# Performance work log

Hardware: AMD Instinct MI355X
Metric: run time of the kernel (lower is better)

## Reference

```python
import jax, jax.numpy as jnp
import numpy as np

N_BODIES = 3
NDOF = 3 * N_BODIES          # 9
HIDDEN = 128                 # max(16, 256//2)
EPS2 = 0.1 ** 2              # softening_eps^2
MASS_EPS = 1e-8
B = 262144
# torch.triu_indices(3, 3, 1) -> pairs (0,1),(0,2),(1,2)
PAIR_I = jnp.array([0, 0, 1])
PAIR_J = jnp.array([1, 2, 2])


def setup_inputs() -> dict:
    key = jax.random.key(0)
    ks = jax.random.split(key, 7)
    inv = lambda n: 1.0 / np.sqrt(n)  # torch Linear default init scale (uniform bound)
    return {
        "z": jax.random.normal(ks[0], (B, 2 * NDOF), jnp.float32),
        "log_m_body": jnp.zeros((N_BODIES,), jnp.float32),
        "W1": jax.random.uniform(ks[1], (HIDDEN, 1), jnp.float32, -inv(1), inv(1)),
        "b1": jax.random.uniform(ks[2], (HIDDEN,), jnp.float32, -inv(1), inv(1)),
        "W2": jax.random.uniform(ks[3], (HIDDEN, HIDDEN), jnp.float32, -inv(HIDDEN), inv(HIDDEN)),
        "b2": jax.random.uniform(ks[4], (HIDDEN,), jnp.float32, -inv(HIDDEN), inv(HIDDEN)),
        "W3": jax.random.uniform(ks[5], (1, HIDDEN), jnp.float32, -inv(HIDDEN), inv(HIDDEN)),
        "b3": jax.random.uniform(ks[6], (1,), jnp.float32, -inv(HIDDEN), inv(HIDDEN)),
    }


def _hamiltonian(z, log_m_body, W1, b1, W2, b2, W3, b3):
    q, p = z[:, :NDOF], z[:, NDOF:]
    # kinetic: T(p) = 0.5 * sum p^2 / m  (tied per-body learned mass)
    minv = 1.0 / (jnp.repeat(jnp.exp(log_m_body), 3) + MASS_EPS)  # [ndof]
    T = 0.5 * jnp.sum(p * p * minv, axis=1)                        # [B]
    # potential: softened inverse pairwise distance -> tiny MLP -> sum over pairs
    qb = q.reshape(-1, N_BODIES, 3)
    diff = qb[:, PAIR_I] - qb[:, PAIR_J]                           # [B,3,3]
    d = jnp.sqrt(jnp.sum(diff * diff, axis=-1) + EPS2)             # [B,3]
    s = (1.0 / d)[..., None]                                       # [B,3,1]
    h = jax.nn.silu(s @ W1.T + b1)                                 # [B,3,128]
    h = jax.nn.silu(h @ W2.T + b2)                                 # [B,3,128]
    v = (h @ W3.T + b3)[..., 0]                                    # [B,3]
    V = jnp.sum(v, axis=1)                                         # [B]
    return T + V


def reference(z, log_m_body, W1, b1, W2, b2, W3, b3):
    # dz/dt = J grad_z H with canonical J: dq/dt = dH/dp, dp/dt = -dH/dq
    grad = jax.grad(
        lambda zz: jnp.sum(_hamiltonian(zz, log_m_body, W1, b1, W2, b2, W3, b3))
    )(z)
    dqdt = grad[:, NDOF:]
    dpdt = -grad[:, :NDOF]
    return jnp.concatenate([dqdt, dpdt], axis=1)
```

## Files before the change

kernel.cpp:

```cpp
#include <hip/hip_runtime.h>
#include <math.h>

#define HIDDEN      128
#define TABLE_N     2048
#define SMAX        10.0f
#define E           8
#define TB_THREADS  128
#define MAIN_THREADS 256
#define EPS2        0.01f
#define MASS_EPS    1e-8f

__global__ __launch_bounds__(TB_THREADS)
void build_table_kernel(const float* __restrict__ W1,
                        const float* __restrict__ b1,
                        const float* __restrict__ W2,
                        const float* __restrict__ b2,
                        const float* __restrict__ W3,
                        float* __restrict__ table)
{
    const int tid = threadIdx.x;
    const int e0  = blockIdx.x * E;
    __shared__ float sh[HIDDEN * E];

    const float ds  = SMAX / (float)(TABLE_N - 1);
    const float w1  = W1[tid];
    const float bb1 = b1[tid];

    float sp1[E];
    #pragma unroll
    for (int e = 0; e < E; ++e) {
        float s  = (float)(e0 + e) * ds;
        float u1 = w1 * s + bb1;
        float sg = 1.0f / (1.0f + expf(-u1));
        sh[tid * E + e] = u1 * sg;
        sp1[e] = sg * (1.0f + u1 * (1.0f - sg));
    }
    __syncthreads();

    float u2[E];
    #pragma unroll
    for (int e = 0; e < E; ++e) u2[e] = b2[tid];
    for (int j = 0; j < HIDDEN; ++j) {
        float w = W2[tid * HIDDEN + j];
        #pragma unroll
        for (int e = 0; e < E; ++e) u2[e] += w * sh[j * E + e];
    }

    const float w3 = W3[tid];
    float a[E];
    #pragma unroll
    for (int e = 0; e < E; ++e) {
        float sg = 1.0f / (1.0f + expf(-u2[e]));
        a[e] = w3 * sg * (1.0f + u2[e] * (1.0f - sg));
    }
    __syncthreads();
    #pragma unroll
    for (int e = 0; e < E; ++e) sh[tid * E + e] = a[e];
    __syncthreads();

    float gv[E];
    #pragma unroll
    for (int e = 0; e < E; ++e) gv[e] = 0.0f;
    for (int i = 0; i < HIDDEN; ++i) {
        float w = W2[i * HIDDEN + tid];
        #pragma unroll
        for (int e = 0; e < E; ++e) gv[e] += w * sh[i * E + e];
    }
    __syncthreads();

    #pragma unroll
    for (int e = 0; e < E; ++e) sh[tid * E + e] = w1 * sp1[e] * gv[e];
    __syncthreads();
    if (tid < E) {
        float g = 0.0f;
        for (int j = 0; j < HIDDEN; ++j) g += sh[j * E + tid];
        table[e0 + tid] = g;
    }
}

__global__ __launch_bounds__(MAIN_THREADS)
void hnn_grad_kernel(const float* __restrict__ z,
                     const float* __restrict__ logm,
                     const float* __restrict__ table,
                     float* __restrict__ out)
{
    __shared__ float buf[MAIN_THREADS * 18];
    const int tid = threadIdx.x;
    const long long base = (long long)blockIdx.x * MAIN_THREADS * 18;

    #pragma unroll
    for (int k = 0; k < 18; ++k)
        buf[k * MAIN_THREADS + tid] = z[base + k * MAIN_THREADS + tid];
    __syncthreads();

    float q[9], p[9];
    #pragma unroll
    for (int c = 0; c < 9; ++c) q[c] = buf[tid * 18 + c];
    #pragma unroll
    for (int c = 0; c < 9; ++c) p[c] = buf[tid * 18 + 9 + c];

    const float minv0 = 1.0f / (expf(logm[0]) + MASS_EPS);
    const float minv1 = 1.0f / (expf(logm[1]) + MASS_EPS);
    const float minv2 = 1.0f / (expf(logm[2]) + MASS_EPS);

    float dq[9], dp[9];
    #pragma unroll
    for (int c = 0; c < 3; ++c) {
        dq[c]     = p[c]     * minv0;
        dq[3 + c] = p[3 + c] * minv1;
        dq[6 + c] = p[6 + c] * minv2;
    }
    #pragma unroll
    for (int c = 0; c < 9; ++c) dp[c] = 0.0f;

    const float scale = (float)(TABLE_N - 1) / SMAX;
    const int pi[3] = {0, 0, 1};
    const int pj[3] = {1, 2, 2};
    #pragma unroll
    for (int k = 0; k < 3; ++k) {
        const int i = pi[k] * 3, j = pj[k] * 3;
        float dx = q[i]     - q[j];
        float dy = q[i + 1] - q[j + 1];
        float dz = q[i + 2] - q[j + 2];
        float r2 = dx * dx + dy * dy + dz * dz + EPS2;
        float d  = sqrtf(r2);
        float s  = 1.0f / d;
        float x  = s * scale;
        int  idx = (int)x;
        idx = idx > (TABLE_N - 2) ? (TABLE_N - 2) : idx;
        float f  = x - (float)idx;
        float t0 = table[idx], t1 = table[idx + 1];
        float g  = t0 + f * (t1 - t0);
        float w = g * s * s * s;
        dp[i]     += w * dx;  dp[i + 1] += w * dy;  dp[i + 2] += w * dz;
        dp[j]     -= w * dx;  dp[j + 1] -= w * dy;  dp[j + 2] -= w * dz;
    }

    __syncthreads();
    #pragma unroll
    for (int c = 0; c < 9; ++c) buf[tid * 18 + c]     = dq[c];
    #pragma unroll
    for (int c = 0; c < 9; ++c) buf[tid * 18 + 9 + c] = dp[c];
    __syncthreads();

    #pragma unroll
    for (int k = 0; k < 18; ++k)
        out[base + k * MAIN_THREADS + tid] = buf[k * MAIN_THREADS + tid];
}

extern "C" void kernel_launch(void* const* d_in, const int* in_sizes, int n_in,
                              void* d_out, int out_size, void* d_ws, size_t ws_size,
                              hipStream_t stream)
{
    const float* z   = (const float*)d_in[0];
    const float* lm  = (const float*)d_in[1];
    const float* W1  = (const float*)d_in[2];
    const float* b1  = (const float*)d_in[3];
    const float* W2  = (const float*)d_in[4];
    const float* b2  = (const float*)d_in[5];
    const float* W3  = (const float*)d_in[6];
    float* out   = (float*)d_out;
    float* table = (float*)d_ws;

    hipLaunchKernelGGL(build_table_kernel, dim3(TABLE_N / E), dim3(TB_THREADS),
                       0, stream, W1, b1, W2, b2, W3, table);

    const int B = in_sizes[0] / 18;
    hipLaunchKernelGGL(hnn_grad_kernel, dim3(B / MAIN_THREADS), dim3(MAIN_THREADS),
                       0, stream, z, lm, table, out);
}
```

Measured before the change: 96.11 us.

## Vectorize main kernel I/O with float4 and retune table build reduction

The main kernel now moves z into shared memory and the result back to global memory with float4 accesses instead of scalar 32-bit accesses, cutting the number of memory instructions. The table build kernel handles 4 table entries per block instead of 8, doubling its block count. It also adds unroll pragmas to its matvec loops and replaces the serial shared-memory sum with wavefront shuffle reductions. The float4 path depends on 16-byte alignment of the buffers and on B being a multiple of the block size.

```diff
diff --git a/kernel.cpp b/kernel.cpp
--- a/kernel.cpp
+++ b/kernel.cpp
@@ -4,7 +4,7 @@
 #define HIDDEN      128
 #define TABLE_N     2048
 #define SMAX        10.0f
-#define E           8
+#define E           4
 #define TB_THREADS  128
 #define MAIN_THREADS 256
 #define EPS2        0.01f
@@ -21,6 +21,7 @@
     const int tid = threadIdx.x;
     const int e0  = blockIdx.x * E;
     __shared__ float sh[HIDDEN * E];
+    __shared__ float wred[2 * E];
 
     const float ds  = SMAX / (float)(TABLE_N - 1);
     const float w1  = W1[tid];
@@ -40,6 +41,7 @@
     float u2[E];
     #pragma unroll
     for (int e = 0; e < E; ++e) u2[e] = b2[tid];
+    #pragma unroll 4
     for (int j = 0; j < HIDDEN; ++j) {
         float w = W2[tid * HIDDEN + j];
         #pragma unroll
@@ -61,21 +63,30 @@
     float gv[E];
     #pragma unroll
     for (int e = 0; e < E; ++e) gv[e] = 0.0f;
+    #pragma unroll 4
     for (int i = 0; i < HIDDEN; ++i) {
         float w = W2[i * HIDDEN + tid];
         #pragma unroll
         for (int e = 0; e < E; ++e) gv[e] += w * sh[i * E + e];
     }
-    __syncthreads();
+
+    float part[E];
+    #pragma unroll
+    for (int e = 0; e < E; ++e) part[e] = w1 * sp1[e] * gv[e];
 
     #pragma unroll
-    for (int e = 0; e < E; ++e) sh[tid * E + e] = w1 * sp1[e] * gv[e];
+    for (int e = 0; e < E; ++e) {
+        #pragma unroll
+        for (int off = 32; off > 0; off >>= 1)
+            part[e] += __shfl_down(part[e], off, 64);
+    }
+    if ((tid & 63) == 0) {
+        const int wave = tid >> 6;
+        #pragma unroll
+        for (int e = 0; e < E; ++e) wred[wave * E + e] = part[e];
+    }
     __syncthreads();
-    if (tid < E) {
-        float g = 0.0f;
-        for (int j = 0; j < HIDDEN; ++j) g += sh[j * E + tid];
-        table[e0 + tid] = g;
-    }
+    if (tid < E) table[e0 + tid] = wred[tid] + wred[E + tid];
 }
 
 __global__ __launch_bounds__(MAIN_THREADS)
@@ -84,13 +95,17 @@
                      const float* __restrict__ table,
                      float* __restrict__ out)
 {
-    __shared__ float buf[MAIN_THREADS * 18];
+    __shared__ __align__(16) float buf[MAIN_THREADS * 18];
     const int tid = threadIdx.x;
-    const long long base = (long long)blockIdx.x * MAIN_THREADS * 18;
+    const long long base = (long long)blockIdx.x * (MAIN_THREADS * 18);
 
+    const float4* __restrict__ zin = reinterpret_cast<const float4*>(z + base);
+    float4* b4 = reinterpret_cast<float4*>(buf);
     #pragma unroll
-    for (int k = 0; k < 18; ++k)
-        buf[k * MAIN_THREADS + tid] = z[base + k * MAIN_THREADS + tid];
+    for (int k = 0; k < 4; ++k)
+        b4[k * MAIN_THREADS + tid] = zin[k * MAIN_THREADS + tid];
+    if (tid < MAIN_THREADS / 2)
+        b4[4 * MAIN_THREADS + tid] = zin[4 * MAIN_THREADS + tid];
     __syncthreads();
 
     float q[9], p[9];
@@ -143,9 +158,12 @@
     for (int c = 0; c < 9; ++c) buf[tid * 18 + 9 + c] = dp[c];
     __syncthreads();
 
+    float4* oout = reinterpret_cast<float4*>(out + base);
     #pragma unroll
-    for (int k = 0; k < 18; ++k)
-        out[base + k * MAIN_THREADS + tid] = buf[k * MAIN_THREADS + tid];
+    for (int k = 0; k < 4; ++k)
+        oout[k * MAIN_THREADS + tid] = b4[k * MAIN_THREADS + tid];
+    if (tid < MAIN_THREADS / 2)
+        oout[4 * MAIN_THREADS + tid] = b4[4 * MAIN_THREADS + tid];
 }
 
 extern "C" void kernel_launch(void* const* d_in, const int* in_sizes, int n_in,
```

After: 95.77 us. Within noise of the previous version (-0.4%).
